# Optimization experiments

Measured on AMD Instinct MI355X. Metric: run time of the kernel, lower is better.

Reference implementation:

```python
import jax, jax.numpy as jnp
import numpy as np

B, S, H, D, DM = 2, 512, 8, 32, 256  # batch, seq_len, n_head, d_k, d_model


def setup_inputs() -> dict:
    key = jax.random.key(0)
    ks = jax.random.split(key, 8)
    scale = 0.02
    return {
        "hidden_states": jax.random.normal(ks[0], (B, S, DM), dtype=jnp.float32),
        "rpe": jax.random.normal(ks[1], (B, S, S, D), dtype=jnp.float32),
        "w_q": jax.random.normal(ks[2], (DM, H * D), dtype=jnp.float32) * scale,
        "w_k": jax.random.normal(ks[3], (DM, H * D), dtype=jnp.float32) * scale,
        "w_v": jax.random.normal(ks[4], (DM, H * D), dtype=jnp.float32) * scale,
        "fc_w": jax.random.normal(ks[5], (H * D, DM), dtype=jnp.float32) * scale,
        "fc_b": jnp.zeros((DM,), dtype=jnp.float32),
        "ln_w": jnp.ones((DM,), dtype=jnp.float32),
        "ln_b": jnp.zeros((DM,), dtype=jnp.float32),
        "station_num": 256,
    }


def reference(hidden_states, rpe, w_q, w_k, w_v, fc_w, fc_b, ln_w, ln_b, station_num):
    b, s, dm = hidden_states.shape
    d = rpe.shape[-1]
    h = w_q.shape[1] // d

    def heads(x, w):
        # (b, s, dm) @ (dm, h*d) -> (b, h, s, d)
        return (x @ w).reshape(b, s, h, d).transpose(0, 2, 1, 3)

    q = heads(hidden_states, w_q)
    k = heads(hidden_states, w_k)
    v = heads(hidden_states, w_v)

    # torch: (q.unsqueeze(2) * k.unsqueeze(3) * rpe.unsqueeze(1)).sum(-1)
    # scores[b,h,i,j] = sum_d q[b,h,j,d] * k[b,h,i,d] * rpe[b,i,j,d]
    scores = jnp.einsum('bhjd,bhid,bijd->bhij', q, k, rpe) / jnp.sqrt(jnp.float32(d))

    # shielded mask: column j visible if j < station_num, plus the diagonal
    col = jnp.arange(s) < station_num                  # (s,)
    mask = col[None, :] | jnp.eye(s, dtype=bool)        # (s, s)
    scores = jnp.where(mask[None, None], scores, jnp.float32(-1e10))

    attn = jax.nn.softmax(scores, axis=-1)              # (b, h, s, s)
    out = jnp.einsum('bhij,bhjd->bhid', attn, v)        # (b, h, s, d)
    out = out.transpose(0, 2, 1, 3).reshape(b, s, h * d)

    ctx = out @ fc_w + fc_b + hidden_states             # residual
    mu = jnp.mean(ctx, axis=-1, keepdims=True)
    var = jnp.mean(jnp.square(ctx - mu), axis=-1, keepdims=True)
    ctx = (ctx - mu) / jnp.sqrt(var + 1e-6) * ln_w + ln_b
    return ctx
```

## Files before the change

### kernel.cpp

```cpp
#include <hip/hip_runtime.h>
#include <hip/hip_bf16.h>

#define B_  2
#define S_  512
#define H_  8
#define D_  32
#define DM_ 256
#define HD_ 256
#define NROW 4
#define TI  2
#define HC  2
#define NR  (TI * HC)
#define JC  32

__global__ __launch_bounds__(256) void qkv_kernel(
    const float* __restrict__ hid, const float* __restrict__ wq,
    const float* __restrict__ wk, const float* __restrict__ wv,
    float* __restrict__ qo, float* __restrict__ ko, float* __restrict__ vo)
{
  __shared__ float hs[NROW][DM_];
  const int r0 = blockIdx.x * NROW;
  const float* w   = (blockIdx.y == 0) ? wq : (blockIdx.y == 1) ? wk : wv;
  float*       out = (blockIdx.y == 0) ? qo : (blockIdx.y == 1) ? ko : vo;
  const float mulf = (blockIdx.y == 0) ? 0.17677669529663687f : 1.0f;
  const int tid = threadIdx.x;

  for (int idx = tid; idx < NROW * DM_; idx += 256)
    hs[idx >> 8][idx & 255] = hid[r0 * DM_ + idx];
  __syncthreads();

  float acc[NROW] = {0.f, 0.f, 0.f, 0.f};
  const float* wp = w + tid;
  #pragma unroll 8
  for (int c4 = 0; c4 < DM_ / 4; ++c4) {
    const float w0 = wp[(4 * c4 + 0) * HD_];
    const float w1 = wp[(4 * c4 + 1) * HD_];
    const float w2 = wp[(4 * c4 + 2) * HD_];
    const float w3 = wp[(4 * c4 + 3) * HD_];
    #pragma unroll
    for (int r = 0; r < NROW; ++r) {
      const float4 hv = reinterpret_cast<const float4*>(&hs[r][0])[c4];
      acc[r] = fmaf(hv.x, w0, acc[r]);
      acc[r] = fmaf(hv.y, w1, acc[r]);
      acc[r] = fmaf(hv.z, w2, acc[r]);
      acc[r] = fmaf(hv.w, w3, acc[r]);
    }
  }
  const int h = tid >> 5, d = tid & 31;
  #pragma unroll
  for (int r = 0; r < NROW; ++r) {
    const int g = r0 + r;
    const int b = g >> 9, s = g & (S_ - 1);
    out[((b * H_ + h) * S_ + s) * D_ + d] = acc[r] * mulf;
  }
}

__device__ __forceinline__ float red8(float x) {
  int i;
  i = __builtin_amdgcn_mov_dpp(__float_as_int(x), 0xB1, 0xf, 0xf, true);
  x += __int_as_float(i);
  i = __builtin_amdgcn_mov_dpp(__float_as_int(x), 0x4E, 0xf, 0xf, true);
  x += __int_as_float(i);
  i = __builtin_amdgcn_mov_dpp(__float_as_int(x), 0x124, 0xf, 0xf, true);
  x += __int_as_float(i);
  return x;
}

__device__ __forceinline__ void lds_dma16(float* dst_uniform, const float* src) {
  __builtin_amdgcn_global_load_lds(
      (const __attribute__((address_space(1))) unsigned int*)src,
      (__attribute__((address_space(3))) unsigned int*)dst_uniform,
      16, 0, 0);
}

__global__ __launch_bounds__(256, 6) void attn_kernel(
    const float* __restrict__ rpe, const float* __restrict__ q_ws,
    const float* __restrict__ k_ws, const float* __restrict__ v_ws,
    const int* __restrict__ station_p, float* __restrict__ o_ws)
{
  __shared__ __align__(16) float rpe_smem[2][TI * JC * D_];
  __shared__ __align__(16) float p_smem[NR * S_];
  __shared__ float sums[NR];

  const int tid  = threadIdx.x;
  const int w    = tid >> 6, lane = tid & 63;
  const int jl   = tid >> 3;
  const int dc   = tid & 7;
  const int j8   = lane >> 3;
  const int n    = blockIdx.x;
  const int hg   = (n >> 3) & 3;
  const int t    = (n & 7) | ((n >> 5) << 3);
  const int b    = t >> 8;
  const int i0   = (t & 255) * TI;
  const int h0   = hg * HC;
  const int HS   = S_ * D_;

  int station = station_p[0];
  station = station > S_ ? S_ : (station < 0 ? 0 : station);
  const int NC = (station + JC - 1) / JC;

  const float* qb = q_ws + (size_t)((b * H_ + h0) * S_) * D_;
  const float* kb = k_ws + (size_t)((b * H_ + h0) * S_ + i0) * D_;
  const float* vb = v_ws + (size_t)((b * H_ + h0) * S_) * D_;
  const float* rb = rpe + ((size_t)b * S_ + i0) * S_ * D_;

  float4 kf[HC][TI];
  #pragma unroll
  for (int hh = 0; hh < HC; ++hh)
    #pragma unroll
    for (int ii = 0; ii < TI; ++ii)
      kf[hh][ii] = *reinterpret_cast<const float4*>(kb + hh * HS + ii * D_ + dc * 4);

  if (NC > 0) {
    #pragma unroll
    for (int it = 0; it < 2; ++it) {
      const int m = w * 2 + it;
      const float* src = rb + (m >> 2) * HS
                       + (size_t)(((m & 3) * 8) + (lane >> 3)) * D_ + (lane & 7) * 4;
      lds_dma16(&rpe_smem[0][m * 256], src);
    }
  }
  __syncthreads();

  for (int c = 0; c < NC; ++c) {
    if (c + 1 < NC) {
      const int jb = (c + 1) * JC;
      #pragma unroll
      for (int it = 0; it < 2; ++it) {
        const int m = w * 2 + it;
        const float* src = rb + (m >> 2) * HS
                         + (size_t)(jb + ((m & 3) * 8) + (lane >> 3)) * D_ + (lane & 7) * 4;
        lds_dma16(&rpe_smem[(c + 1) & 1][m * 256], src);
      }
    }
    const float* buf = rpe_smem[c & 1];
    const int j = c * JC + jl;
    const float4 rv0 = *reinterpret_cast<const float4*>(buf + tid * 4);
    const float4 rv1 = *reinterpret_cast<const float4*>(buf + (256 + tid) * 4);
    const float4 q0 = *reinterpret_cast<const float4*>(qb + (size_t)j * D_ + dc * 4);
    const float4 q1 = *reinterpret_cast<const float4*>(qb + HS + (size_t)j * D_ + dc * 4);
    const bool st = (dc == 0) && (j < station);

    float s;
    s = q0.x * kf[0][0].x * rv0.x;
    s = fmaf(q0.y * kf[0][0].y, rv0.y, s);
    s = fmaf(q0.z * kf[0][0].z, rv0.z, s);
    s = fmaf(q0.w * kf[0][0].w, rv0.w, s);
    s = red8(s);
    if (st) p_smem[0 * S_ + j] = s;

    s = q0.x * kf[0][1].x * rv1.x;
    s = fmaf(q0.y * kf[0][1].y, rv1.y, s);
    s = fmaf(q0.z * kf[0][1].z, rv1.z, s);
    s = fmaf(q0.w * kf[0][1].w, rv1.w, s);
    s = red8(s);
    if (st) p_smem[1 * S_ + j] = s;

    s = q1.x * kf[1][0].x * rv0.x;
    s = fmaf(q1.y * kf[1][0].y, rv0.y, s);
    s = fmaf(q1.z * kf[1][0].z, rv0.z, s);
    s = fmaf(q1.w * kf[1][0].w, rv0.w, s);
    s = red8(s);
    if (st) p_smem[2 * S_ + j] = s;

    s = q1.x * kf[1][1].x * rv1.x;
    s = fmaf(q1.y * kf[1][1].y, rv1.y, s);
    s = fmaf(q1.z * kf[1][1].z, rv1.z, s);
    s = fmaf(q1.w * kf[1][1].w, rv1.w, s);
    s = red8(s);
    if (st) p_smem[3 * S_ + j] = s;

    __syncthreads();
  }

  if (w == 0 && lane < TI * 8) {
    const int ii = lane >> 3;
    const int j = i0 + ii;
    if (j >= station) {
      const float4 rv = *reinterpret_cast<const float4*>(
          rb + ii * HS + (size_t)j * D_ + dc * 4);
      #pragma unroll
      for (int hh = 0; hh < HC; ++hh) {
        const float4 q4 = *reinterpret_cast<const float4*>(
            qb + hh * HS + (size_t)j * D_ + dc * 4);
        const float4 k4 = *reinterpret_cast<const float4*>(
            kb + hh * HS + ii * D_ + dc * 4);
        float s = q4.x * k4.x * rv.x;
        s = fmaf(q4.y * k4.y, rv.y, s);
        s = fmaf(q4.z * k4.z, rv.z, s);
        s = fmaf(q4.w * k4.w, rv.w, s);
        s = red8(s);
        if (dc == 0) p_smem[(hh * TI + ii) * S_ + j] = s;
      }
    }
  }
  __syncthreads();

  {
    const int r  = w;
    const int ii = r & (TI - 1);
    const int ig = i0 + ii;
    const bool dx = (ig >= station);
    float m = -1e30f;
    for (int jj = lane; jj < station; jj += 64) m = fmaxf(m, p_smem[r * S_ + jj]);
    const float dv = dx ? p_smem[r * S_ + ig] : -1e30f;
    m = fmaxf(m, dv);
    #pragma unroll
    for (int o = 32; o; o >>= 1) m = fmaxf(m, __shfl_xor(m, o, 64));
    float sum = 0.f;
    for (int jj = lane; jj < station; jj += 64) {
      const float e = __expf(p_smem[r * S_ + jj] - m);
      p_smem[r * S_ + jj] = e;
      sum += e;
    }
    #pragma unroll
    for (int o = 32; o; o >>= 1) sum += __shfl_xor(sum, o, 64);
    if (dx) {
      const float e = __expf(dv - m);
      sum += e;
      if (lane == 0) p_smem[r * S_ + ig] = e;
    }
    if (lane == 0) sums[r] = sum;
  }
  __syncthreads();

  float4 acc[HC][TI];
  #pragma unroll
  for (int hh = 0; hh < HC; ++hh)
    #pragma unroll
    for (int ii = 0; ii < TI; ++ii) acc[hh][ii] = make_float4(0.f, 0.f, 0.f, 0.f);

  for (int jb = w * 8; jb < station; jb += 32) {
    const int j  = jb + j8;
    const int jc = j < S_ ? j : S_ - 1;
    float4 v4[HC];
    #pragma unroll
    for (int hh = 0; hh < HC; ++hh)
      v4[hh] = *reinterpret_cast<const float4*>(vb + hh * HS + jc * D_ + dc * 4);
    #pragma unroll
    for (int hh = 0; hh < HC; ++hh)
      #pragma unroll
      for (int ii = 0; ii < TI; ++ii) {
        float pv = 0.f;
        if (j < station) pv = p_smem[(hh * TI + ii) * S_ + j];
        acc[hh][ii].x = fmaf(pv, v4[hh].x, acc[hh][ii].x);
        acc[hh][ii].y = fmaf(pv, v4[hh].y, acc[hh][ii].y);
        acc[hh][ii].z = fmaf(pv, v4[hh].z, acc[hh][ii].z);
        acc[hh][ii].w = fmaf(pv, v4[hh].w, acc[hh][ii].w);
      }
  }
  if (w == 0 && j8 == 0) {
    #pragma unroll
    for (int ii = 0; ii < TI; ++ii) {
      const int ig = i0 + ii;
      if (ig >= station) {
        #pragma unroll
        for (int hh = 0; hh < HC; ++hh) {
          const float pv = p_smem[(hh * TI + ii) * S_ + ig];
          const float4 v4 = *reinterpret_cast<const float4*>(vb + hh * HS + ig * D_ + dc * 4);
          acc[hh][ii].x = fmaf(pv, v4.x, acc[hh][ii].x);
          acc[hh][ii].y = fmaf(pv, v4.y, acc[hh][ii].y);
          acc[hh][ii].z = fmaf(pv, v4.z, acc[hh][ii].z);
          acc[hh][ii].w = fmaf(pv, v4.w, acc[hh][ii].w);
        }
      }
    }
  }
  __syncthreads();

  float4* redv = reinterpret_cast<float4*>(p_smem);
  #pragma unroll
  for (int hh = 0; hh < HC; ++hh)
    #pragma unroll
    for (int ii = 0; ii < TI; ++ii) {
      const int r = hh * TI + ii;
      float4 a = acc[hh][ii];
      a.x += __shfl_xor(a.x, 8);
      a.y += __shfl_xor(a.y, 8);
      a.z += __shfl_xor(a.z, 8);
      a.w += __shfl_xor(a.w, 8);
      if ((j8 & 1) == 0)
        redv[((w * 4 + (j8 >> 1)) * NR + r) * 8 + dc] = a;
    }
  __syncthreads();
  if (tid < NR * 8) {
    const int r = tid >> 3, d4 = tid & 7;
    float4 a = make_float4(0.f, 0.f, 0.f, 0.f);
    #pragma unroll
    for (int g = 0; g < 16; ++g) {
      const float4 x = redv[(g * NR + r) * 8 + d4];
      a.x += x.x; a.y += x.y; a.z += x.z; a.w += x.w;
    }
    const float inv = 1.f / sums[r];
    a.x *= inv; a.y *= inv; a.z *= inv; a.w *= inv;
    const int hh = r >> 1, ii = r & 1;
    reinterpret_cast<float4*>(
        o_ws + (size_t)((b * H_ + h0 + hh) * S_ + i0 + ii) * D_)[d4] = a;
  }
}

__global__ __launch_bounds__(256) void fc_ln_kernel(
    const float* __restrict__ o_ws, const float* __restrict__ fc_w,
    const float* __restrict__ fc_b, const float* __restrict__ hid,
    const float* __restrict__ ln_w, const float* __restrict__ ln_b,
    float* __restrict__ out)
{
  __shared__ float orow[NROW][HD_];
  __shared__ float red[NROW][4];
  const int tid = threadIdx.x;
  const int r0 = blockIdx.x * NROW;

  for (int idx = tid; idx < NROW * HD_; idx += 256) {
    const int r = idx >> 8, m = idx & 255;
    const int g = r0 + r;
    const int b = g >> 9, i = g & (S_ - 1);
    orow[r][m] = o_ws[((b * H_ + (m >> 5)) * S_ + i) * D_ + (m & 31)];
  }
  __syncthreads();

  float acc[NROW] = {0.f, 0.f, 0.f, 0.f};
  const float* wp = fc_w + tid;
  #pragma unroll 8
  for (int n4 = 0; n4 < HD_ / 4; ++n4) {
    const float w0 = wp[(4 * n4 + 0) * DM_];
    const float w1 = wp[(4 * n4 + 1) * DM_];
    const float w2 = wp[(4 * n4 + 2) * DM_];
    const float w3 = wp[(4 * n4 + 3) * DM_];
    #pragma unroll
    for (int r = 0; r < NROW; ++r) {
      const float4 ov = reinterpret_cast<const float4*>(&orow[r][0])[n4];
      acc[r] = fmaf(ov.x, w0, acc[r]);
      acc[r] = fmaf(ov.y, w1, acc[r]);
      acc[r] = fmaf(ov.z, w2, acc[r]);
      acc[r] = fmaf(ov.w, w3, acc[r]);
    }
  }
  const float bias = fc_b[tid];
  #pragma unroll
  for (int r = 0; r < NROW; ++r) acc[r] += bias + hid[(r0 + r) * DM_ + tid];

  const int w = tid >> 6, lane = tid & 63;
  float mu[NROW];
  #pragma unroll
  for (int r = 0; r < NROW; ++r) {
    float s = acc[r];
    #pragma unroll
    for (int o = 32; o; o >>= 1) s += __shfl_xor(s, o, 64);
    if (lane == 0) red[r][w] = s;
  }
  __syncthreads();
  #pragma unroll
  for (int r = 0; r < NROW; ++r)
    mu[r] = (red[r][0] + red[r][1] + red[r][2] + red[r][3]) * (1.f / DM_);
  __syncthreads();
  #pragma unroll
  for (int r = 0; r < NROW; ++r) {
    const float dd = acc[r] - mu[r];
    float s = dd * dd;
    #pragma unroll
    for (int o = 32; o; o >>= 1) s += __shfl_xor(s, o, 64);
    if (lane == 0) red[r][w] = s;
  }
  __syncthreads();
  const float lw = ln_w[tid], lb = ln_b[tid];
  #pragma unroll
  for (int r = 0; r < NROW; ++r) {
    const float var = (red[r][0] + red[r][1] + red[r][2] + red[r][3]) * (1.f / DM_);
    out[(r0 + r) * DM_ + tid] =
        (acc[r] - mu[r]) * rsqrtf(var + 1e-6f) * lw + lb;
  }
}

extern "C" void kernel_launch(void* const* d_in, const int* in_sizes, int n_in,
                              void* d_out, int out_size, void* d_ws, size_t ws_size,
                              hipStream_t stream) {
  const float* hid = (const float*)d_in[0];
  const float* rpe = (const float*)d_in[1];
  const float* wq  = (const float*)d_in[2];
  const float* wk  = (const float*)d_in[3];
  const float* wv  = (const float*)d_in[4];
  const float* fcw = (const float*)d_in[5];
  const float* fcb = (const float*)d_in[6];
  const float* lnw = (const float*)d_in[7];
  const float* lnb = (const float*)d_in[8];
  const int* station = (const int*)d_in[9];
  float* out = (float*)d_out;

  const size_t per = (size_t)B_ * H_ * S_ * D_;
  float* q_ws = (float*)d_ws;
  float* k_ws = q_ws + per;
  float* v_ws = k_ws + per;
  float* o_ws = v_ws + per;

  dim3 gA(B_ * S_ / NROW, 3);
  qkv_kernel<<<gA, 256, 0, stream>>>(hid, wq, wk, wv, q_ws, k_ws, v_ws);
  attn_kernel<<<B_ * (S_ / TI) * (H_ / HC), 256, 0, stream>>>(
      rpe, q_ws, k_ws, v_ws, station, o_ws);
  fc_ln_kernel<<<B_ * S_ / NROW, 256, 0, stream>>>(o_ws, fcw, fcb, hid, lnw, lnb, out);
}
```

Baseline: 159.5 us.

## Replace block-synchronous rpe double buffer with per-wave 4-deep async LDS ring

Each wave now owns a private 4-slot LDS ring. It streams rpe and q tiles with global_load_lds DMA and paces itself with s_waitcnt vmcnt, which removes the per-chunk __syncthreads that every wave used to hit. The k fragments are staged through LDS, and q also moves into the async path instead of direct global loads. The aim is more loads in flight and no block-wide barriers in the score loop. The cost is much more LDS per block, and launch bounds drop from 6 to 2 blocks per CU, which lowers occupancy.

```diff
diff --git a/kernel.cpp b/kernel.cpp
--- a/kernel.cpp
+++ b/kernel.cpp
@@ -11,7 +11,7 @@
 #define TI  2
 #define HC  2
 #define NR  (TI * HC)
-#define JC  32
+#define DEPTH 4
 
 __global__ __launch_bounds__(256) void qkv_kernel(
     const float* __restrict__ hid, const float* __restrict__ wq,
@@ -73,20 +73,19 @@
       16, 0, 0);
 }
 
-__global__ __launch_bounds__(256, 6) void attn_kernel(
+__global__ __launch_bounds__(256, 2) void attn_kernel(
     const float* __restrict__ rpe, const float* __restrict__ q_ws,
     const float* __restrict__ k_ws, const float* __restrict__ v_ws,
     const int* __restrict__ station_p, float* __restrict__ o_ws)
 {
-  __shared__ __align__(16) float rpe_smem[2][TI * JC * D_];
+  __shared__ __align__(16) float ring[4 * DEPTH * 1024];
   __shared__ __align__(16) float p_smem[NR * S_];
+  __shared__ __align__(16) float k_lds[HC * TI * D_];
   __shared__ float sums[NR];
 
   const int tid  = threadIdx.x;
   const int w    = tid >> 6, lane = tid & 63;
-  const int jl   = tid >> 3;
-  const int dc   = tid & 7;
-  const int j8   = lane >> 3;
+  const int j8   = lane >> 3, dc = lane & 7;
   const int n    = blockIdx.x;
   const int hg   = (n >> 3) & 3;
   const int t    = (n & 7) | ((n >> 5) << 3);
@@ -97,80 +96,88 @@
 
   int station = station_p[0];
   station = station > S_ ? S_ : (station < 0 ? 0 : station);
-  const int NC = (station + JC - 1) / JC;
 
   const float* qb = q_ws + (size_t)((b * H_ + h0) * S_) * D_;
   const float* kb = k_ws + (size_t)((b * H_ + h0) * S_ + i0) * D_;
   const float* vb = v_ws + (size_t)((b * H_ + h0) * S_) * D_;
   const float* rb = rpe + ((size_t)b * S_ + i0) * S_ * D_;
 
-  float4 kf[HC][TI];
-  #pragma unroll
-  for (int hh = 0; hh < HC; ++hh)
-    #pragma unroll
-    for (int ii = 0; ii < TI; ++ii)
-      kf[hh][ii] = *reinterpret_cast<const float4*>(kb + hh * HS + ii * D_ + dc * 4);
-
-  if (NC > 0) {
-    #pragma unroll
-    for (int it = 0; it < 2; ++it) {
-      const int m = w * 2 + it;
-      const float* src = rb + (m >> 2) * HS
-                       + (size_t)(((m & 3) * 8) + (lane >> 3)) * D_ + (lane & 7) * 4;
-      lds_dma16(&rpe_smem[0][m * 256], src);
-    }
-  }
-  __syncthreads();
-
-  for (int c = 0; c < NC; ++c) {
-    if (c + 1 < NC) {
-      const int jb = (c + 1) * JC;
-      #pragma unroll
-      for (int it = 0; it < 2; ++it) {
-        const int m = w * 2 + it;
-        const float* src = rb + (m >> 2) * HS
-                         + (size_t)(jb + ((m & 3) * 8) + (lane >> 3)) * D_ + (lane & 7) * 4;
-        lds_dma16(&rpe_smem[(c + 1) & 1][m * 256], src);
-      }
-    }
-    const float* buf = rpe_smem[c & 1];
-    const int j = c * JC + jl;
-    const float4 rv0 = *reinterpret_cast<const float4*>(buf + tid * 4);
-    const float4 rv1 = *reinterpret_cast<const float4*>(buf + (256 + tid) * 4);
-    const float4 q0 = *reinterpret_cast<const float4*>(qb + (size_t)j * D_ + dc * 4);
-    const float4 q1 = *reinterpret_cast<const float4*>(qb + HS + (size_t)j * D_ + dc * 4);
-    const bool st = (dc == 0) && (j < station);
-
-    float s;
-    s = q0.x * kf[0][0].x * rv0.x;
-    s = fmaf(q0.y * kf[0][0].y, rv0.y, s);
-    s = fmaf(q0.z * kf[0][0].z, rv0.z, s);
-    s = fmaf(q0.w * kf[0][0].w, rv0.w, s);
-    s = red8(s);
-    if (st) p_smem[0 * S_ + j] = s;
-
-    s = q0.x * kf[0][1].x * rv1.x;
-    s = fmaf(q0.y * kf[0][1].y, rv1.y, s);
-    s = fmaf(q0.z * kf[0][1].z, rv1.z, s);
-    s = fmaf(q0.w * kf[0][1].w, rv1.w, s);
-    s = red8(s);
-    if (st) p_smem[1 * S_ + j] = s;
-
-    s = q1.x * kf[1][0].x * rv0.x;
-    s = fmaf(q1.y * kf[1][0].y, rv0.y, s);
-    s = fmaf(q1.z * kf[1][0].z, rv0.z, s);
-    s = fmaf(q1.w * kf[1][0].w, rv0.w, s);
-    s = red8(s);
-    if (st) p_smem[2 * S_ + j] = s;
-
-    s = q1.x * kf[1][1].x * rv1.x;
-    s = fmaf(q1.y * kf[1][1].y, rv1.y, s);
-    s = fmaf(q1.z * kf[1][1].z, rv1.z, s);
-    s = fmaf(q1.w * kf[1][1].w, rv1.w, s);
-    s = red8(s);
-    if (st) p_smem[3 * S_ + j] = s;
-
-    __syncthreads();
+  if (tid < HC * TI * D_) k_lds[tid] = kb[((tid >> 5) & 1) * HS +
+                                         0];
+  if (tid < HC * TI * D_) {
+    const int hh = tid / (TI * D_);
+    const int rem = tid - hh * (TI * D_);
+    const int ii = rem / D_, d = rem - ii * D_;
+    k_lds[tid] = kb[hh * HS + ii * D_ + d];
+  }
+  __syncthreads();
+
+  float4 kf00, kf01, kf10, kf11;
+  kf00 = *reinterpret_cast<const float4*>(&k_lds[(0 * TI + 0) * D_ + dc * 4]);
+  kf01 = *reinterpret_cast<const float4*>(&k_lds[(0 * TI + 1) * D_ + dc * 4]);
+  kf10 = *reinterpret_cast<const float4*>(&k_lds[(1 * TI + 0) * D_ + dc * 4]);
+  kf11 = *reinterpret_cast<const float4*>(&k_lds[(1 * TI + 1) * D_ + dc * 4]);
+
+  const int myj0 = w * 8;
+  const int NCW  = (station > myj0) ? ((station - myj0 + 31) >> 5) : 0;
+  float* slotb = ring + w * (DEPTH * 1024);
+
+  auto issue = [&](int c) {
+    const int jbase = myj0 + c * 32;
+    int jl = jbase + j8;
+    jl = jl < S_ ? jl : S_ - 1;
+    const size_t boff = (size_t)jl * D_ + dc * 4;
+    float* dst = slotb + (c & (DEPTH - 1)) * 1024;
+    lds_dma16(dst + 0,   rb + 0 * HS + boff);
+    lds_dma16(dst + 256, rb + 1 * HS + boff);
+    lds_dma16(dst + 512, qb + 0 * HS + boff);
+    lds_dma16(dst + 768, qb + 1 * HS + boff);
+  };
+
+  if (NCW > 0) {
+    #pragma unroll
+    for (int s = 0; s < DEPTH; ++s) issue(s < NCW ? s : NCW - 1);
+    for (int c = 0; c < NCW; ++c) {
+      asm volatile("s_waitcnt vmcnt(12)" ::: "memory");
+      const float* slot = slotb + (c & (DEPTH - 1)) * 1024;
+      const float4 rv0 = *reinterpret_cast<const float4*>(slot +   0 + lane * 4);
+      const float4 rv1 = *reinterpret_cast<const float4*>(slot + 256 + lane * 4);
+      const float4 q0  = *reinterpret_cast<const float4*>(slot + 512 + lane * 4);
+      const float4 q1  = *reinterpret_cast<const float4*>(slot + 768 + lane * 4);
+      const int j = myj0 + c * 32 + j8;
+      const bool st = (dc == 0) && (j < station);
+
+      float s0 = q0.x * kf00.x * rv0.x;
+      s0 = fmaf(q0.y * kf00.y, rv0.y, s0);
+      s0 = fmaf(q0.z * kf00.z, rv0.z, s0);
+      s0 = fmaf(q0.w * kf00.w, rv0.w, s0);
+      s0 = red8(s0);
+      if (st) p_smem[0 * S_ + j] = s0;
+
+      float s1 = q0.x * kf01.x * rv1.x;
+      s1 = fmaf(q0.y * kf01.y, rv1.y, s1);
+      s1 = fmaf(q0.z * kf01.z, rv1.z, s1);
+      s1 = fmaf(q0.w * kf01.w, rv1.w, s1);
+      s1 = red8(s1);
+      if (st) p_smem[1 * S_ + j] = s1;
+
+      float s2 = q1.x * kf10.x * rv0.x;
+      s2 = fmaf(q1.y * kf10.y, rv0.y, s2);
+      s2 = fmaf(q1.z * kf10.z, rv0.z, s2);
+      s2 = fmaf(q1.w * kf10.w, rv0.w, s2);
+      s2 = red8(s2);
+      if (st) p_smem[2 * S_ + j] = s2;
+
+      float s3 = q1.x * kf11.x * rv1.x;
+      s3 = fmaf(q1.y * kf11.y, rv1.y, s3);
+      s3 = fmaf(q1.z * kf11.z, rv1.z, s3);
+      s3 = fmaf(q1.w * kf11.w, rv1.w, s3);
+      s3 = red8(s3);
+      if (st) p_smem[3 * S_ + j] = s3;
+
+      const int cn = c + DEPTH;
+      issue(cn < NCW ? cn : NCW - 1);
+    }
   }
 
   if (w == 0 && lane < TI * 8) {
```

After: 173.6 us. 8.8% more time.
